# Performance work log

Measured on AMD Instinct MI355X. Metric: run time of the kernel, lower is better.

The kernel has to match this reference:

```python
import jax, jax.numpy as jnp
import numpy as np

B, T, D, H, L = 128, 512, 512, 512, 256


def setup_inputs() -> dict:
    key = jax.random.key(0)
    ks = jax.random.split(key, 7)
    lim = 1.0 / np.sqrt(H)
    u = lambda k, shape, lo: jax.random.uniform(k, shape, jnp.float32, -lo, lo)
    x = jax.random.normal(ks[0], (B, T, D), dtype=jnp.float32)
    Wih = u(ks[1], (3 * H, D), lim)
    Whh = u(ks[2], (3 * H, H), lim)
    b = u(ks[3], (3 * H,), lim)
    bn = u(ks[4], (H,), lim)
    lim_l = 1.0 / np.sqrt(H)
    Wlin = u(ks[5], (2 * L, H), lim_l)
    blin = u(ks[6], (2 * L,), lim_l)
    return {"x": x, "Wih": Wih, "Whh": Whh, "b": b, "bn": bn, "Wlin": Wlin, "blin": blin}


def reference(x, Wih, Whh, b, bn, Wlin, blin):
    # x: (B, T, D). Batched GRU recurrence over time via lax.scan.
    def step(h, xt):
        ig = xt @ Wih.T + b           # (B, 3H)
        hg = h @ Whh.T                # (B, 3H)
        ir, iz, inn = jnp.split(ig, 3, axis=-1)
        hr, hz, hn = jnp.split(hg, 3, axis=-1)
        r = jax.nn.sigmoid(ir + hr)
        z = jax.nn.sigmoid(iz + hz)
        n = jnp.tanh(inn + r * (hn + bn))
        h_new = (1.0 - z) * n + z * h
        return h_new, None

    xs = jnp.swapaxes(x, 0, 1)        # (T, B, D)
    h0 = jnp.zeros((x.shape[0], Whh.shape[1]), dtype=x.dtype)
    h_final, _ = jax.lax.scan(step, h0, xs)
    out = h_final @ Wlin.T + blin     # (B, 2L)
    mu, logvar = jnp.split(out, 2, axis=-1)
    return (mu, logvar)
```

## Files before the change

kernel.cpp:

```cpp
#include <hip/hip_runtime.h>
#include <stdint.h>


typedef short short8 __attribute__((ext_vector_type(8)));
typedef float f32x4 __attribute__((ext_vector_type(4)));
typedef int int4v __attribute__((ext_vector_type(4)));

#define NB 128
#define NT 512
#define ND 512
#define NH 512
#define NG 1536
#define HSLOT (NB * NH)

__device__ __forceinline__ unsigned short f2bf(float f) {
  union { float f; unsigned u; } v; v.f = f;
  unsigned r = v.u + 0x7fffu + ((v.u >> 16) & 1u);
  return (unsigned short)(r >> 16);
}
__device__ __forceinline__ float bf2f(unsigned short u) {
  union { unsigned u; float f; } v; v.u = ((unsigned)u) << 16; return v.f;
}
__device__ __forceinline__ float sigmoid_f(float x) {
  float e = __builtin_amdgcn_exp2f(-1.4426950408889634f * x);
  return __builtin_amdgcn_rcpf(1.0f + e);
}
__device__ __forceinline__ float tanh_f(float x) {
  float e = __builtin_amdgcn_exp2f(2.8853900817779268f * x);
  return 1.0f - 2.0f * __builtin_amdgcn_rcpf(1.0f + e);
}
__device__ __forceinline__ short8 pack8(float4 a, float4 b) {
  short8 s;
  s[0] = (short)f2bf(a.x); s[1] = (short)f2bf(a.y);
  s[2] = (short)f2bf(a.z); s[3] = (short)f2bf(a.w);
  s[4] = (short)f2bf(b.x); s[5] = (short)f2bf(b.y);
  s[6] = (short)f2bf(b.z); s[7] = (short)f2bf(b.w);
  return s;
}

__device__ __forceinline__ int4v load16_s(const unsigned short* p) {
  int4v v;
  asm volatile("global_load_dwordx4 %0, %1, off sc0 sc1\n\t"
               "s_waitcnt vmcnt(0)"
               : "=v"(v) : "v"(p) : "memory");
  return v;
}

__device__ __forceinline__ void load16x4_s(const unsigned short* p0,
                                           const unsigned short* p1,
                                           const unsigned short* p2,
                                           const unsigned short* p3,
                                           int4v* v0, int4v* v1,
                                           int4v* v2, int4v* v3) {
  asm volatile(
      "global_load_dwordx4 %0, %4, off sc0 sc1\n\t"
      "global_load_dwordx4 %1, %5, off sc0 sc1\n\t"
      "global_load_dwordx4 %2, %6, off sc0 sc1\n\t"
      "global_load_dwordx4 %3, %7, off sc0 sc1\n\t"
      "s_waitcnt vmcnt(0)"
      : "=&v"(*v0), "=&v"(*v1), "=&v"(*v2), "=&v"(*v3)
      : "v"(p0), "v"(p1), "v"(p2), "v"(p3) : "memory");
}

__device__ __forceinline__ void store8_nd(unsigned short* p, unsigned long long v) {
  asm volatile("global_store_dwordx2 %0, %1, off sc0 sc1"
               :: "v"(p), "v"(v) : "memory");
}

__device__ __forceinline__ unsigned pkmax(unsigned a, unsigned b) {
  unsigned d;
  asm("v_pk_max_u16 %0, %1, %2" : "=v"(d) : "v"(a), "v"(b));
  return d;
}
__device__ __forceinline__ bool has_sent(int4v v) {
  unsigned m = pkmax(pkmax((unsigned)v[0], (unsigned)v[1]),
                     pkmax((unsigned)v[2], (unsigned)v[3]));
  return ((m & 0xFFFFu) == 0xFFFFu) || ((m >> 16) == 0xFFFFu);
}

__global__ __launch_bounds__(256) void ig_gemm(
    const float* __restrict__ x, const float* __restrict__ Wih,
    const float* __restrict__ bias, unsigned short* __restrict__ IG) {
  __shared__ unsigned short As[128 * 40];
  __shared__ unsigned short Bs[128 * 40];
  const int tid = threadIdx.x;
  const int bn = blockIdx.x, bm = blockIdx.y;
  const int lane = tid & 63, w = tid >> 6;
  const int wm = w >> 1, wn = w & 1;
  const int l15 = lane & 15, q = lane >> 4;

  f32x4 acc[4][4] = {};

  for (int kt = 0; kt < 16; ++kt) {
    __syncthreads();
#pragma unroll
    for (int j = 0; j < 4; ++j) {
      int fi = tid + 256 * j;
      int row = fi >> 3, kq = fi & 7;
      float4 v = *(const float4*)(x + (size_t)(bm * 128 + row) * ND + kt * 32 + kq * 4);
      ushort4 s = {f2bf(v.x), f2bf(v.y), f2bf(v.z), f2bf(v.w)};
      *(ushort4*)&As[row * 40 + kq * 4] = s;
    }
#pragma unroll
    for (int j = 0; j < 4; ++j) {
      int fi = tid + 256 * j;
      int row = fi >> 3, kq = fi & 7;
      float4 v = *(const float4*)(Wih + (size_t)(bn * 128 + row) * ND + kt * 32 + kq * 4);
      ushort4 s = {f2bf(v.x), f2bf(v.y), f2bf(v.z), f2bf(v.w)};
      *(ushort4*)&Bs[row * 40 + kq * 4] = s;
    }
    __syncthreads();

    short8 af[4], bf[4];
#pragma unroll
    for (int tm = 0; tm < 4; ++tm)
      af[tm] = *(const short8*)&As[(wm * 64 + tm * 16 + l15) * 40 + q * 8];
#pragma unroll
    for (int tn = 0; tn < 4; ++tn)
      bf[tn] = *(const short8*)&Bs[(wn * 64 + tn * 16 + l15) * 40 + q * 8];
#pragma unroll
    for (int tm = 0; tm < 4; ++tm)
#pragma unroll
      for (int tn = 0; tn < 4; ++tn)
        acc[tm][tn] = __builtin_amdgcn_mfma_f32_16x16x32_bf16(af[tm], bf[tn], acc[tm][tn], 0, 0, 0);
  }

#pragma unroll
  for (int tm = 0; tm < 4; ++tm) {
#pragma unroll
    for (int tn = 0; tn < 4; ++tn) {
      int col = bn * 128 + wn * 64 + tn * 16 + l15;
      float bb = bias[col];
#pragma unroll
      for (int i = 0; i < 4; ++i) {
        int row = bm * 128 + wm * 64 + tm * 16 + q * 4 + i;
        IG[(size_t)row * NG + col] = f2bf(acc[tm][tn][i] + bb);
      }
    }
  }
}

template <bool USE_IG>
__global__ __launch_bounds__(256, 1) void gru_rec(
    const float* __restrict__ x, const float* __restrict__ Wih,
    const float* __restrict__ Whh, const float* __restrict__ bias,
    const float* __restrict__ bn, const unsigned short* __restrict__ IG,
    unsigned short* __restrict__ hbuf, float* __restrict__ hfin) {
  __shared__ unsigned short hs[16 * 512];
  __shared__ unsigned short ts[16 * 64];

  const int tid = threadIdx.x;
  const int lane = tid & 63;
  const int w = tid >> 6;
  const int l15 = lane & 15, q = lane >> 4;
  const int bid = blockIdx.x;
  const int g = bid & 7, c = bid >> 3;
  const int col = c * 64 + w * 16 + l15;
  const int erow = g * 16 + q * 4;
  const int mrow = g * 16 + l15;

  short8 bfr[3][16];
#pragma unroll
  for (int gt = 0; gt < 3; ++gt) {
    const float* src = Whh + (size_t)(gt * NH + col) * NH + q * 8;
#pragma unroll
    for (int kk = 0; kk < 16; ++kk) {
      float4 v0 = *(const float4*)(src + kk * 32);
      float4 v1 = *(const float4*)(src + kk * 32 + 4);
      bfr[gt][kk] = pack8(v0, v1);
    }
  }

  float bi_r = 0.f, bi_z = 0.f, bi_n = 0.f;
  if (!USE_IG) {
    bi_r = bias[col];
    bi_z = bias[NH + col];
    bi_n = bias[2 * NH + col];
  }
  const float bnv = bn[col];

  float hreg[4] = {0.f, 0.f, 0.f, 0.f};

  const int frow = tid >> 4;
  const int fg0 = (tid & 15) * 4;
  const int fr7 = frow & 7;
  const bool own_slot = ((fg0 >> 3) == c);

  const int srow = tid >> 4;
  const int scol = (tid & 15) * 4;
  const size_t cell_off = (size_t)(g * 16 + srow) * NH + c * 64 + scol;

  for (int t = 0; t < NT; ++t) {
    const unsigned short* hcur = hbuf + (size_t)(t & 3) * HSLOT;
    unsigned short* hnxt  = hbuf + (size_t)((t + 1) & 3) * HSLOT;
    unsigned short* hsent = hbuf + (size_t)((t + 2) & 3) * HSLOT;

    float igr[4], igz[4], ign[4];
    if (USE_IG) {
#pragma unroll
      for (int i = 0; i < 4; ++i) {
        const size_t base = ((size_t)(erow + i) * NT + t) * NG + col;
        igr[i] = bf2f(IG[base]);
        igz[i] = bf2f(IG[base + NH]);
        ign[i] = bf2f(IG[base + 2 * NH]);
      }
    }

    if (t > 0 && own_slot) {
#pragma unroll
      for (int j = 0; j < 4; ++j) {
        const int s = fg0 + j;
        const int ls = (s ^ fr7) & 7;
        *(int4v*)&hs[frow * 512 + (s << 3)] =
            *(const int4v*)&ts[frow * 64 + ls * 8];
      }
    } else {
      const unsigned short* hrow = hcur + (size_t)(g * 16 + frow) * NH;
      const unsigned short* p0 = hrow + (((fg0 + 0) ^ fr7) << 3);
      const unsigned short* p1 = hrow + (((fg0 + 1) ^ fr7) << 3);
      const unsigned short* p2 = hrow + (((fg0 + 2) ^ fr7) << 3);
      const unsigned short* p3 = hrow + (((fg0 + 3) ^ fr7) << 3);
      int4v v0, v1, v2, v3;
      load16x4_s(p0, p1, p2, p3, &v0, &v1, &v2, &v3);
      if (t > 0) {
        while (has_sent(v0)) v0 = load16_s(p0);
        while (has_sent(v1)) v1 = load16_s(p1);
        while (has_sent(v2)) v2 = load16_s(p2);
        while (has_sent(v3)) v3 = load16_s(p3);
      }
      *(int4v*)&hs[frow * 512 + ((fg0 + 0) << 3)] = v0;
      *(int4v*)&hs[frow * 512 + ((fg0 + 1) << 3)] = v1;
      *(int4v*)&hs[frow * 512 + ((fg0 + 2) << 3)] = v2;
      *(int4v*)&hs[frow * 512 + ((fg0 + 3) << 3)] = v3;
    }
    __syncthreads();

    if (t + 2 < NT) {
      store8_nd(hsent + cell_off, 0xFFFFFFFFFFFFFFFFull);
    }

    f32x4 ar = {0.f, 0.f, 0.f, 0.f};
    f32x4 az = {0.f, 0.f, 0.f, 0.f};
    f32x4 an = {0.f, 0.f, 0.f, 0.f};
    f32x4 ai = {0.f, 0.f, 0.f, 0.f};
    const int abase = l15 * 512;
    const int ar7 = (l15 & 7) << 3;
#pragma unroll
    for (int kk = 0; kk < 16; ++kk) {
      short8 afk = *(const short8*)&hs[abase + ((kk * 32 + q * 8) ^ ar7)];
      ar = __builtin_amdgcn_mfma_f32_16x16x32_bf16(afk, bfr[0][kk], ar, 0, 0, 0);
      az = __builtin_amdgcn_mfma_f32_16x16x32_bf16(afk, bfr[1][kk], az, 0, 0, 0);
      an = __builtin_amdgcn_mfma_f32_16x16x32_bf16(afk, bfr[2][kk], an, 0, 0, 0);
      if (!USE_IG) {
        const float* xp = x + ((size_t)mrow * NT + t) * ND + kk * 32 + q * 8;
        short8 xa = pack8(*(const float4*)xp, *(const float4*)(xp + 4));
#pragma unroll
        for (int gt = 0; gt < 3; ++gt) {
          const float* wp = Wih + (size_t)(gt * NH + col) * ND + kk * 32 + q * 8;
          short8 wf = pack8(*(const float4*)wp, *(const float4*)(wp + 4));
          if (gt == 0) ar = __builtin_amdgcn_mfma_f32_16x16x32_bf16(xa, wf, ar, 0, 0, 0);
          if (gt == 1) az = __builtin_amdgcn_mfma_f32_16x16x32_bf16(xa, wf, az, 0, 0, 0);
          if (gt == 2) ai = __builtin_amdgcn_mfma_f32_16x16x32_bf16(xa, wf, ai, 0, 0, 0);
        }
      }
    }

    unsigned short sv[4];
#pragma unroll
    for (int i = 0; i < 4; ++i) {
      float xr = USE_IG ? (ar[i] + igr[i]) : (ar[i] + bi_r);
      float xz = USE_IG ? (az[i] + igz[i]) : (az[i] + bi_z);
      float xin = USE_IG ? ign[i] : (ai[i] + bi_n);
      float r = sigmoid_f(xr);
      float z = sigmoid_f(xz);
      float n = tanh_f(xin + r * (an[i] + bnv));
      float hn2 = (1.f - z) * n + z * hreg[i];
      hreg[i] = hn2;
      sv[i] = f2bf(hn2);
      if (t == NT - 1) hfin[(size_t)(erow + i) * NH + col] = hn2;
    }

    if (t != NT - 1) {
#pragma unroll
      for (int i = 0; i < 4; ++i)
        ts[(q * 4 + i) * 64 + w * 16 + l15] = sv[i];
      asm volatile("s_waitcnt vmcnt(0)" ::: "memory");
      __syncthreads();
      unsigned long long v8 = *(const unsigned long long*)&ts[srow * 64 + scol];
      store8_nd(hnxt + cell_off, v8);
    }
  }
}

__global__ __launch_bounds__(256) void final_linear(
    const float* __restrict__ hfin, const float* __restrict__ Wlin,
    const float* __restrict__ blin, float* __restrict__ out) {
  __shared__ float sh[16 * 516];
  const int tid = threadIdx.x;
  const int b0 = blockIdx.y * 16, o0 = blockIdx.x * 16;

  for (int j = tid; j < 16 * 128; j += 256) {
    int row = j >> 7, kq = j & 127;
    *(float4*)&sh[row * 516 + kq * 4] =
        *(const float4*)(hfin + (size_t)(b0 + row) * NH + kq * 4);
  }
  __syncthreads();

  const int bi = tid & 15, oi = tid >> 4;
  const int o = o0 + oi;
  const float4* wp = (const float4*)(Wlin + (size_t)o * NH);
  float4 a4 = {0.f, 0.f, 0.f, 0.f};
  for (int k4 = 0; k4 < 128; ++k4) {
    float4 wv = wp[k4];
    float4 hv = *(const float4*)&sh[bi * 516 + k4 * 4];
    a4.x += wv.x * hv.x; a4.y += wv.y * hv.y;
    a4.z += wv.z * hv.z; a4.w += wv.w * hv.w;
  }
  float v = a4.x + a4.y + a4.z + a4.w + blin[o];
  int b = b0 + bi;
  if (o < 256) out[b * 256 + o] = v;
  else out[32768 + b * 256 + (o - 256)] = v;
}

extern "C" void kernel_launch(void* const* d_in, const int* in_sizes, int n_in,
                              void* d_out, int out_size, void* d_ws, size_t ws_size,
                              hipStream_t stream) {
  const float* x    = (const float*)d_in[0];
  const float* Wih  = (const float*)d_in[1];
  const float* Whh  = (const float*)d_in[2];
  const float* bias = (const float*)d_in[3];
  const float* bn   = (const float*)d_in[4];
  const float* Wlin = (const float*)d_in[5];
  const float* blin = (const float*)d_in[6];
  float* out = (float*)d_out;

  char* ws = (char*)d_ws;
  unsigned short* hbuf = (unsigned short*)ws;
  float* hfin          = (float*)(ws + 4 * 131072);
  unsigned short* IG   = (unsigned short*)(ws + 4 * 131072 + 262144);
  const size_t need_min = 4 * 131072 + 262144;
  const size_t need_ig  = need_min + (size_t)NB * NT * NG * 2;
  if (ws_size < need_min) return;

  hipMemsetAsync(ws, 0, 131072, stream);
  hipMemsetAsync(ws + 131072, 0xFF, 3 * 131072, stream);

  const bool useIG = (ws_size >= need_ig);
  if (useIG) {
    ig_gemm<<<dim3(12, 512), 256, 0, stream>>>(x, Wih, bias, IG);
    gru_rec<true><<<64, 256, 0, stream>>>(x, Wih, Whh, bias, bn, IG, hbuf, hfin);
  } else {
    gru_rec<false><<<64, 256, 0, stream>>>(x, Wih, Whh, bias, bn, nullptr, hbuf, hfin);
  }
  final_linear<<<dim3(32, 8), 256, 0, stream>>>(hfin, Wlin, blin, out);
}
```

Baseline: 2.079 ms.

## Interleave two batch groups per block to overlap h-exchange latency with compute

The recurrent kernel now gives each block two 16-row batch groups and alternates between them, so the global loads of one group's hidden state are issued before computing the other group. This is meant to hide the cross-block hidden-state exchange latency behind MFMA work. It halves the grid to 32 blocks and drops the local shared-memory shortcut for the block's own slice, so every slice is now read through global memory. The cost is fewer active CUs and two sync phases per timestep.

```diff
diff --git a/kernel.cpp b/kernel.cpp
--- a/kernel.cpp
+++ b/kernel.cpp
@@ -38,28 +38,27 @@
   return s;
 }
 
+__device__ __forceinline__ void issue16x4(const unsigned short* p, int4v (&v)[4]) {
+  asm volatile(
+      "global_load_dwordx4 %0, %4, off sc0 sc1\n\t"
+      "global_load_dwordx4 %1, %4, off offset:256 sc0 sc1\n\t"
+      "global_load_dwordx4 %2, %4, off offset:512 sc0 sc1\n\t"
+      "global_load_dwordx4 %3, %4, off offset:768 sc0 sc1"
+      : "=&v"(v[0]), "=&v"(v[1]), "=&v"(v[2]), "=&v"(v[3])
+      : "v"(p) : "memory");
+}
+
+__device__ __forceinline__ void wait4(int4v (&v)[4]) {
+  asm volatile("s_waitcnt vmcnt(0)"
+               : "+v"(v[0]), "+v"(v[1]), "+v"(v[2]), "+v"(v[3]) :: "memory");
+}
+
 __device__ __forceinline__ int4v load16_s(const unsigned short* p) {
   int4v v;
   asm volatile("global_load_dwordx4 %0, %1, off sc0 sc1\n\t"
                "s_waitcnt vmcnt(0)"
                : "=v"(v) : "v"(p) : "memory");
   return v;
-}
-
-__device__ __forceinline__ void load16x4_s(const unsigned short* p0,
-                                           const unsigned short* p1,
-                                           const unsigned short* p2,
-                                           const unsigned short* p3,
-                                           int4v* v0, int4v* v1,
-                                           int4v* v2, int4v* v3) {
-  asm volatile(
-      "global_load_dwordx4 %0, %4, off sc0 sc1\n\t"
-      "global_load_dwordx4 %1, %5, off sc0 sc1\n\t"
-      "global_load_dwordx4 %2, %6, off sc0 sc1\n\t"
-      "global_load_dwordx4 %3, %7, off sc0 sc1\n\t"
-      "s_waitcnt vmcnt(0)"
-      : "=&v"(*v0), "=&v"(*v1), "=&v"(*v2), "=&v"(*v3)
-      : "v"(p0), "v"(p1), "v"(p2), "v"(p3) : "memory");
 }
 
 __device__ __forceinline__ void store8_nd(unsigned short* p, unsigned long long v) {
@@ -141,23 +140,137 @@
 }
 
 template <bool USE_IG>
+__device__ __forceinline__ void gru_phase(
+    int t, int rbase, unsigned short* __restrict__ ts,
+    int t_nxt, int rbase_nxt, bool issue_nxt,
+    int4v (&v)[4],
+    const float* __restrict__ x, const float* __restrict__ Wih,
+    const unsigned short* __restrict__ IG,
+    unsigned short* __restrict__ hbuf, float* __restrict__ hfin,
+    unsigned short* __restrict__ hs,
+    const short8 (&bfr)[3][16], float (&hreg)[4],
+    float bi_r, float bi_z, float bi_n, float bnv,
+    int tid, int w, int l15, int q, int c) {
+  const int col = c * 64 + w * 16 + l15;
+  const int erow = rbase + q * 4;
+  const int mrow = rbase + l15;
+
+  const int frow = tid >> 4;
+  const int k15 = tid & 15;
+  const int fr7 = frow & 7;
+  const int gbase = (k15 ^ fr7) << 3;
+
+  const int srow = frow;
+  const int scol = k15 * 4;
+  const size_t cell_off = (size_t)(rbase + srow) * NH + c * 64 + scol;
+
+  float igr[4], igz[4], ign[4];
+  if (USE_IG) {
+#pragma unroll
+    for (int i = 0; i < 4; ++i) {
+      const size_t base = ((size_t)(erow + i) * NT + t) * NG + col;
+      igr[i] = bf2f(IG[base]);
+      igz[i] = bf2f(IG[base + NH]);
+      ign[i] = bf2f(IG[base + 2 * NH]);
+    }
+  }
+
+  {
+    const unsigned short* hrow =
+        hbuf + (size_t)(t & 3) * HSLOT + (size_t)(rbase + frow) * NH;
+    if (t > 0) {
+#pragma unroll
+      for (int j = 0; j < 4; ++j)
+        while (has_sent(v[j])) v[j] = load16_s(hrow + gbase + j * 128);
+    }
+#pragma unroll
+    for (int j = 0; j < 4; ++j)
+      *(int4v*)&hs[frow * 512 + k15 * 8 + j * 128] = v[j];
+  }
+  __syncthreads();
+
+  if (t + 2 < NT)
+    store8_nd(hbuf + (size_t)((t + 2) & 3) * HSLOT + cell_off,
+              0xFFFFFFFFFFFFFFFFull);
+  if (issue_nxt) {
+    const unsigned short* hrow_n =
+        hbuf + (size_t)(t_nxt & 3) * HSLOT + (size_t)(rbase_nxt + frow) * NH;
+    issue16x4(hrow_n + gbase, v);
+  }
+
+  f32x4 ar = {0.f, 0.f, 0.f, 0.f};
+  f32x4 az = {0.f, 0.f, 0.f, 0.f};
+  f32x4 an = {0.f, 0.f, 0.f, 0.f};
+  f32x4 ai = {0.f, 0.f, 0.f, 0.f};
+  const int abase = l15 * 512;
+  const int ar7 = (l15 & 7) << 3;
+#pragma unroll
+  for (int kk = 0; kk < 16; ++kk) {
+    short8 afk = *(const short8*)&hs[abase + ((kk * 32 + q * 8) ^ ar7)];
+    ar = __builtin_amdgcn_mfma_f32_16x16x32_bf16(afk, bfr[0][kk], ar, 0, 0, 0);
+    az = __builtin_amdgcn_mfma_f32_16x16x32_bf16(afk, bfr[1][kk], az, 0, 0, 0);
+    an = __builtin_amdgcn_mfma_f32_16x16x32_bf16(afk, bfr[2][kk], an, 0, 0, 0);
+    if (!USE_IG) {
+      const float* xp = x + ((size_t)mrow * NT + t) * ND + kk * 32 + q * 8;
+      short8 xa = pack8(*(const float4*)xp, *(const float4*)(xp + 4));
+#pragma unroll
+      for (int gt = 0; gt < 3; ++gt) {
+        const float* wp = Wih + (size_t)(gt * NH + col) * ND + kk * 32 + q * 8;
+        short8 wf = pack8(*(const float4*)wp, *(const float4*)(wp + 4));
+        if (gt == 0) ar = __builtin_amdgcn_mfma_f32_16x16x32_bf16(xa, wf, ar, 0, 0, 0);
+        if (gt == 1) az = __builtin_amdgcn_mfma_f32_16x16x32_bf16(xa, wf, az, 0, 0, 0);
+        if (gt == 2) ai = __builtin_amdgcn_mfma_f32_16x16x32_bf16(xa, wf, ai, 0, 0, 0);
+      }
+    }
+  }
+
+  unsigned short sv[4];
+#pragma unroll
+  for (int i = 0; i < 4; ++i) {
+    float xr = USE_IG ? (ar[i] + igr[i]) : (ar[i] + bi_r);
+    float xz = USE_IG ? (az[i] + igz[i]) : (az[i] + bi_z);
+    float xin = USE_IG ? ign[i] : (ai[i] + bi_n);
+    float r = sigmoid_f(xr);
+    float z = sigmoid_f(xz);
+    float n = tanh_f(xin + r * (an[i] + bnv));
+    float hn2 = (1.f - z) * n + z * hreg[i];
+    hreg[i] = hn2;
+    sv[i] = f2bf(hn2);
+    if (t == NT - 1) hfin[(size_t)(erow + i) * NH + col] = hn2;
+  }
+
+  if (t != NT - 1) {
+#pragma unroll
+    for (int i = 0; i < 4; ++i)
+      ts[(q * 4 + i) * 64 + w * 16 + l15] = sv[i];
+    wait4(v);
+    __syncthreads();
+    store8_nd(hbuf + (size_t)((t + 1) & 3) * HSLOT + cell_off,
+              *(const unsigned long long*)&ts[srow * 64 + scol]);
+  } else {
+    wait4(v);
+    __syncthreads();
+  }
+}
+
+template <bool USE_IG>
 __global__ __launch_bounds__(256, 1) void gru_rec(
     const float* __restrict__ x, const float* __restrict__ Wih,
     const float* __restrict__ Whh, const float* __restrict__ bias,
     const float* __restrict__ bn, const unsigned short* __restrict__ IG,
     unsigned short* __restrict__ hbuf, float* __restrict__ hfin) {
-  __shared__ unsigned short hs[16 * 512];
-  __shared__ unsigned short ts[16 * 64];
+  __shared__ __align__(16) unsigned short hs[16 * 512];
+  __shared__ __align__(16) unsigned short tsA[16 * 64];
+  __shared__ __align__(16) unsigned short tsB[16 * 64];
 
   const int tid = threadIdx.x;
   const int lane = tid & 63;
   const int w = tid >> 6;
   const int l15 = lane & 15, q = lane >> 4;
   const int bid = blockIdx.x;
-  const int g = bid & 7, c = bid >> 3;
+  const int p = bid >> 3, c = bid & 7;
+  const int rbA = p * 32, rbB = p * 32 + 16;
   const int col = c * 64 + w * 16 + l15;
-  const int erow = g * 16 + q * 4;
-  const int mrow = g * 16 + l15;
 
   short8 bfr[3][16];
 #pragma unroll
@@ -179,116 +292,23 @@
   }
   const float bnv = bn[col];
 
-  float hreg[4] = {0.f, 0.f, 0.f, 0.f};
-
-  const int frow = tid >> 4;
-  const int fg0 = (tid & 15) * 4;
-  const int fr7 = frow & 7;
-  const bool own_slot = ((fg0 >> 3) == c);
-
-  const int srow = tid >> 4;
-  const int scol = (tid & 15) * 4;
-  const size_t cell_off = (size_t)(g * 16 + srow) * NH + c * 64 + scol;
+  float hregA[4] = {0.f, 0.f, 0.f, 0.f};
+  float hregB[4] = {0.f, 0.f, 0.f, 0.f};
+
+  int4v v[4];
+  {
+    const int frow = tid >> 4, k15 = tid & 15, fr7 = frow & 7;
+    const unsigned short* hrow = hbuf + (size_t)(rbA + frow) * NH;
+    issue16x4(hrow + ((k15 ^ fr7) << 3), v);
+    wait4(v);
+  }
 
   for (int t = 0; t < NT; ++t) {
-    const unsigned short* hcur = hbuf + (size_t)(t & 3) * HSLOT;
-    unsigned short* hnxt  = hbuf + (size_t)((t + 1) & 3) * HSLOT;
-    unsigned short* hsent = hbuf + (size_t)((t + 2) & 3) * HSLOT;
-
-    float igr[4], igz[4], ign[4];
-    if (USE_IG) {
-#pragma unroll
-      for (int i = 0; i < 4; ++i) {
-        const size_t base = ((size_t)(erow + i) * NT + t) * NG + col;
-        igr[i] = bf2f(IG[base]);
-        igz[i] = bf2f(IG[base + NH]);
-        ign[i] = bf2f(IG[base + 2 * NH]);
-      }
-    }
-
-    if (t > 0 && own_slot) {
-#pragma unroll
-      for (int j = 0; j < 4; ++j) {
-        const int s = fg0 + j;
-        const int ls = (s ^ fr7) & 7;
-        *(int4v*)&hs[frow * 512 + (s << 3)] =
-            *(const int4v*)&ts[frow * 64 + ls * 8];
-      }
-    } else {
-      const unsigned short* hrow = hcur + (size_t)(g * 16 + frow) * NH;
-      const unsigned short* p0 = hrow + (((fg0 + 0) ^ fr7) << 3);
-      const unsigned short* p1 = hrow + (((fg0 + 1) ^ fr7) << 3);
-      const unsigned short* p2 = hrow + (((fg0 + 2) ^ fr7) << 3);
-      const unsigned short* p3 = hrow + (((fg0 + 3) ^ fr7) << 3);
-      int4v v0, v1, v2, v3;
-      load16x4_s(p0, p1, p2, p3, &v0, &v1, &v2, &v3);
-      if (t > 0) {
-        while (has_sent(v0)) v0 = load16_s(p0);
-        while (has_sent(v1)) v1 = load16_s(p1);
-        while (has_sent(v2)) v2 = load16_s(p2);
-        while (has_sent(v3)) v3 = load16_s(p3);
-      }
-      *(int4v*)&hs[frow * 512 + ((fg0 + 0) << 3)] = v0;
-      *(int4v*)&hs[frow * 512 + ((fg0 + 1) << 3)] = v1;
-      *(int4v*)&hs[frow * 512 + ((fg0 + 2) << 3)] = v2;
-      *(int4v*)&hs[frow * 512 + ((fg0 + 3) << 3)] = v3;
-    }
-    __syncthreads();
-
-    if (t + 2 < NT) {
-      store8_nd(hsent + cell_off, 0xFFFFFFFFFFFFFFFFull);
-    }
-
-    f32x4 ar = {0.f, 0.f, 0.f, 0.f};
-    f32x4 az = {0.f, 0.f, 0.f, 0.f};
-    f32x4 an = {0.f, 0.f, 0.f, 0.f};
-    f32x4 ai = {0.f, 0.f, 0.f, 0.f};
-    const int abase = l15 * 512;
-    const int ar7 = (l15 & 7) << 3;
-#pragma unroll
-    for (int kk = 0; kk < 16; ++kk) {
-      short8 afk = *(const short8*)&hs[abase + ((kk * 32 + q * 8) ^ ar7)];
-      ar = __builtin_amdgcn_mfma_f32_16x16x32_bf16(afk, bfr[0][kk], ar, 0, 0, 0);
-      az = __builtin_amdgcn_mfma_f32_16x16x32_bf16(afk, bfr[1][kk], az, 0, 0, 0);
-      an = __builtin_amdgcn_mfma_f32_16x16x32_bf16(afk, bfr[2][kk], an, 0, 0, 0);
-      if (!USE_IG) {
-        const float* xp = x + ((size_t)mrow * NT + t) * ND + kk * 32 + q * 8;
-        short8 xa = pack8(*(const float4*)xp, *(const float4*)(xp + 4));
-#pragma unroll
-        for (int gt = 0; gt < 3; ++gt) {
-          const float* wp = Wih + (size_t)(gt * NH + col) * ND + kk * 32 + q * 8;
-          short8 wf = pack8(*(const float4*)wp, *(const float4*)(wp + 4));
-          if (gt == 0) ar = __builtin_amdgcn_mfma_f32_16x16x32_bf16(xa, wf, ar, 0, 0, 0);
-          if (gt == 1) az = __builtin_amdgcn_mfma_f32_16x16x32_bf16(xa, wf, az, 0, 0, 0);
-          if (gt == 2) ai = __builtin_amdgcn_mfma_f32_16x16x32_bf16(xa, wf, ai, 0, 0, 0);
-        }
-      }
-    }
-
-    unsigned short sv[4];
-#pragma unroll
-    for (int i = 0; i < 4; ++i) {
-      float xr = USE_IG ? (ar[i] + igr[i]) : (ar[i] + bi_r);
-      float xz = USE_IG ? (az[i] + igz[i]) : (az[i] + bi_z);
-      float xin = USE_IG ? ign[i] : (ai[i] + bi_n);
-      float r = sigmoid_f(xr);
-      float z = sigmoid_f(xz);
-      float n = tanh_f(xin + r * (an[i] + bnv));
-      float hn2 = (1.f - z) * n + z * hreg[i];
-      hreg[i] = hn2;
-      sv[i] = f2bf(hn2);
-      if (t == NT - 1) hfin[(size_t)(erow + i) * NH + col] = hn2;
-    }
-
-    if (t != NT - 1) {
-#pragma unroll
-      for (int i = 0; i < 4; ++i)
-        ts[(q * 4 + i) * 64 + w * 16 + l15] = sv[i];
-      asm volatile("s_waitcnt vmcnt(0)" ::: "memory");
-      __syncthreads();
-      unsigned long long v8 = *(const unsigned long long*)&ts[srow * 64 + scol];
-      store8_nd(hnxt + cell_off, v8);
-    }
+    gru_phase<USE_IG>(t, rbA, tsA, t, rbB, true, v, x, Wih, IG, hbuf, hfin,
+                      hs, bfr, hregA, bi_r, bi_z, bi_n, bnv, tid, w, l15, q, c);
+    gru_phase<USE_IG>(t, rbB, tsB, t + 1, rbA, (t + 1) < NT, v, x, Wih, IG,
+                      hbuf, hfin, hs, bfr, hregB, bi_r, bi_z, bi_n, bnv,
+                      tid, w, l15, q, c);
   }
 }
 
@@ -348,9 +368,9 @@
   const bool useIG = (ws_size >= need_ig);
   if (useIG) {
     ig_gemm<<<dim3(12, 512), 256, 0, stream>>>(x, Wih, bias, IG);
-    gru_rec<true><<<64, 256, 0, stream>>>(x, Wih, Whh, bias, bn, IG, hbuf, hfin);
+    gru_rec<true><<<32, 256, 0, stream>>>(x, Wih, Whh, bias, bn, IG, hbuf, hfin);
   } else {
-    gru_rec<false><<<64, 256, 0, stream>>>(x, Wih, Whh, bias, bn, nullptr, hbuf, hfin);
+    gru_rec<false><<<32, 256, 0, stream>>>(x, Wih, Whh, bias, bn, nullptr, hbuf, hfin);
   }
   final_linear<<<dim3(32, 8), 256, 0, stream>>>(hfin, Wlin, blin, out);
 }
```

Measured after the change: 2.261 ms. 1.09x slower.

## Prefetch next hidden state right after publishing, drop own-slot LDS path

Applied to the files above, without the earlier changes.

The recurrent kernel now issues the global loads for the next step's hidden-state row immediately after storing its own slice, and waits for them only at the top of the next iteration. The intent is to overlap the cross-block polling latency with the loop overhead and the IG loads. It also changes the slot mapping so each thread reads strided chunks, and it removes the shortcut that copied the block's own slice from LDS. The cost is that every chunk, including the block's own, now goes through global memory. The early prefetch may also pick up sentinel values and need extra spin reloads.

```diff
diff --git a/kernel.cpp b/kernel.cpp
--- a/kernel.cpp
+++ b/kernel.cpp
@@ -38,28 +38,31 @@
   return s;
 }
 
+__device__ __forceinline__ void issue4(const unsigned short* r0,
+                                       const unsigned short* r1,
+                                       const unsigned short* r2,
+                                       const unsigned short* r3,
+                                       int4v (&v)[4]) {
+  asm volatile(
+      "global_load_dwordx4 %0, %4, off sc0 sc1\n\t"
+      "global_load_dwordx4 %1, %5, off sc0 sc1\n\t"
+      "global_load_dwordx4 %2, %6, off sc0 sc1\n\t"
+      "global_load_dwordx4 %3, %7, off sc0 sc1"
+      : "=&v"(v[0]), "=&v"(v[1]), "=&v"(v[2]), "=&v"(v[3])
+      : "v"(r0), "v"(r1), "v"(r2), "v"(r3) : "memory");
+}
+
+__device__ __forceinline__ void wait4(int4v (&v)[4]) {
+  asm volatile("s_waitcnt vmcnt(0)"
+               : "+v"(v[0]), "+v"(v[1]), "+v"(v[2]), "+v"(v[3]) :: "memory");
+}
+
 __device__ __forceinline__ int4v load16_s(const unsigned short* p) {
   int4v v;
   asm volatile("global_load_dwordx4 %0, %1, off sc0 sc1\n\t"
                "s_waitcnt vmcnt(0)"
                : "=v"(v) : "v"(p) : "memory");
   return v;
-}
-
-__device__ __forceinline__ void load16x4_s(const unsigned short* p0,
-                                           const unsigned short* p1,
-                                           const unsigned short* p2,
-                                           const unsigned short* p3,
-                                           int4v* v0, int4v* v1,
-                                           int4v* v2, int4v* v3) {
-  asm volatile(
-      "global_load_dwordx4 %0, %4, off sc0 sc1\n\t"
-      "global_load_dwordx4 %1, %5, off sc0 sc1\n\t"
-      "global_load_dwordx4 %2, %6, off sc0 sc1\n\t"
-      "global_load_dwordx4 %3, %7, off sc0 sc1\n\t"
-      "s_waitcnt vmcnt(0)"
-      : "=&v"(*v0), "=&v"(*v1), "=&v"(*v2), "=&v"(*v3)
-      : "v"(p0), "v"(p1), "v"(p2), "v"(p3) : "memory");
 }
 
 __device__ __forceinline__ void store8_nd(unsigned short* p, unsigned long long v) {
@@ -146,8 +149,8 @@
     const float* __restrict__ Whh, const float* __restrict__ bias,
     const float* __restrict__ bn, const unsigned short* __restrict__ IG,
     unsigned short* __restrict__ hbuf, float* __restrict__ hfin) {
-  __shared__ unsigned short hs[16 * 512];
-  __shared__ unsigned short ts[16 * 64];
+  __shared__ __align__(16) unsigned short hs[16 * 512];
+  __shared__ __align__(16) unsigned short ts[16 * 64];
 
   const int tid = threadIdx.x;
   const int lane = tid & 63;
@@ -182,18 +185,27 @@
   float hreg[4] = {0.f, 0.f, 0.f, 0.f};
 
   const int frow = tid >> 4;
-  const int fg0 = (tid & 15) * 4;
+  const int j2 = tid & 15;
   const int fr7 = frow & 7;
-  const bool own_slot = ((fg0 >> 3) == c);
+  const size_t rowoff = (size_t)(g * 16 + frow) * NH;
+  const int e0 = ((j2) ^ fr7) << 3;
+  const int e1 = ((j2 + 16) ^ fr7) << 3;
+  const int e2 = ((32 + j2) ^ fr7) << 3;
+  const int e3 = ((48 + j2) ^ fr7) << 3;
 
   const int srow = tid >> 4;
   const int scol = (tid & 15) * 4;
   const size_t cell_off = (size_t)(g * 16 + srow) * NH + c * 64 + scol;
+
+  int4v v[4];
+  issue4(hbuf + rowoff + e0, hbuf + rowoff + e1,
+         hbuf + rowoff + e2, hbuf + rowoff + e3, v);
 
   for (int t = 0; t < NT; ++t) {
     const unsigned short* hcur = hbuf + (size_t)(t & 3) * HSLOT;
     unsigned short* hnxt  = hbuf + (size_t)((t + 1) & 3) * HSLOT;
     unsigned short* hsent = hbuf + (size_t)((t + 2) & 3) * HSLOT;
+    const unsigned short* hrow = hcur + rowoff;
 
     float igr[4], igz[4], ign[4];
     if (USE_IG) {
@@ -206,38 +218,20 @@
       }
     }
 
-    if (t > 0 && own_slot) {
-#pragma unroll
-      for (int j = 0; j < 4; ++j) {
-        const int s = fg0 + j;
-        const int ls = (s ^ fr7) & 7;
-        *(int4v*)&hs[frow * 512 + (s << 3)] =
-            *(const int4v*)&ts[frow * 64 + ls * 8];
-      }
-    } else {
-      const unsigned short* hrow = hcur + (size_t)(g * 16 + frow) * NH;
-      const unsigned short* p0 = hrow + (((fg0 + 0) ^ fr7) << 3);
-      const unsigned short* p1 = hrow + (((fg0 + 1) ^ fr7) << 3);
-      const unsigned short* p2 = hrow + (((fg0 + 2) ^ fr7) << 3);
-      const unsigned short* p3 = hrow + (((fg0 + 3) ^ fr7) << 3);
-      int4v v0, v1, v2, v3;
-      load16x4_s(p0, p1, p2, p3, &v0, &v1, &v2, &v3);
-      if (t > 0) {
-        while (has_sent(v0)) v0 = load16_s(p0);
-        while (has_sent(v1)) v1 = load16_s(p1);
-        while (has_sent(v2)) v2 = load16_s(p2);
-        while (has_sent(v3)) v3 = load16_s(p3);
-      }
-      *(int4v*)&hs[frow * 512 + ((fg0 + 0) << 3)] = v0;
-      *(int4v*)&hs[frow * 512 + ((fg0 + 1) << 3)] = v1;
-      *(int4v*)&hs[frow * 512 + ((fg0 + 2) << 3)] = v2;
-      *(int4v*)&hs[frow * 512 + ((fg0 + 3) << 3)] = v3;
-    }
+    wait4(v);
+    if (t > 0) {
+      while (has_sent(v[0])) v[0] = load16_s(hrow + e0);
+      while (has_sent(v[1])) v[1] = load16_s(hrow + e1);
+      while (has_sent(v[2])) v[2] = load16_s(hrow + e2);
+      while (has_sent(v[3])) v[3] = load16_s(hrow + e3);
+    }
+    *(int4v*)&hs[frow * 512 + (j2 << 3)] = v[0];
+    *(int4v*)&hs[frow * 512 + ((j2 + 16) << 3)] = v[1];
+    *(int4v*)&hs[frow * 512 + ((32 + j2) << 3)] = v[2];
+    *(int4v*)&hs[frow * 512 + ((48 + j2) << 3)] = v[3];
     __syncthreads();
 
-    if (t + 2 < NT) {
-      store8_nd(hsent + cell_off, 0xFFFFFFFFFFFFFFFFull);
-    }
+    if (t + 2 < NT) store8_nd(hsent + cell_off, 0xFFFFFFFFFFFFFFFFull);
 
     f32x4 ar = {0.f, 0.f, 0.f, 0.f};
     f32x4 az = {0.f, 0.f, 0.f, 0.f};
@@ -286,8 +280,10 @@
         ts[(q * 4 + i) * 64 + w * 16 + l15] = sv[i];
       asm volatile("s_waitcnt vmcnt(0)" ::: "memory");
       __syncthreads();
-      unsigned long long v8 = *(const unsigned long long*)&ts[srow * 64 + scol];
-      store8_nd(hnxt + cell_off, v8);
+      store8_nd(hnxt + cell_off,
+                *(const unsigned long long*)&ts[srow * 64 + scol]);
+      issue4(hnxt + rowoff + e0, hnxt + rowoff + e1,
+             hnxt + rowoff + e2, hnxt + rowoff + e3, v);
     }
   }
 }
```

Result: no change. 2.060 ms (-0.9%).
